# Performance work log

Hardware: AMD Instinct MI355X
Metric: run time of the kernel (lower is better)

## Reference

```python
import jax, jax.numpy as jnp
import numpy as np

EPS = 1e-5
B, C, H, W, K = 4, 512, 128, 128, 32


def setup_inputs() -> dict:
    key = jax.random.key(0)
    ks = jax.random.split(key, 12)
    std = 1.0 / ((K * C) ** 0.5)
    return {
        "x": jax.random.normal(ks[0], (B, C, H, W), jnp.float32),
        "conv_w": jax.random.normal(ks[1], (C, C), jnp.float32) * (1.0 / C ** 0.5),
        "bn2_g": jnp.ones((C,), jnp.float32),
        "bn2_b": jnp.zeros((C,), jnp.float32),
        "bn2_m": jax.random.normal(ks[2], (C,), jnp.float32) * 0.1,
        "bn2_v": jax.random.uniform(ks[3], (C,), jnp.float32) + 0.5,
        "codewords": jax.random.uniform(ks[4], (K, C), jnp.float32, -std, std),
        "scale": jax.random.uniform(ks[5], (K,), jnp.float32, -1.0, 0.0),
        "bn1_g": jnp.ones((K,), jnp.float32),
        "bn1_b": jnp.zeros((K,), jnp.float32),
        "bn1_m": jax.random.normal(ks[6], (K,), jnp.float32) * 0.1,
        "bn1_v": jax.random.uniform(ks[7], (K,), jnp.float32) + 0.5,
        "fc_w": jax.random.normal(ks[8], (C, C), jnp.float32) * (1.0 / C ** 0.5),
        "fc_b": jnp.zeros((C,), jnp.float32),
    }


def _encoding(z, codewords, scale):
    # z: [B,N,C], codewords: [K,C], scale: [K]
    # scaled L2: scale_k * ||z_n - c_k||^2, expanded to avoid the [B,N,K,C] tensor
    x2 = jnp.sum(z * z, axis=-1, keepdims=True)          # [B,N,1]
    c2 = jnp.sum(codewords * codewords, axis=-1)         # [K]
    xc = jnp.einsum('bnc,kc->bnk', z, codewords)         # [B,N,K]
    scaled_l2 = scale * (x2 - 2.0 * xc + c2)             # [B,N,K]
    assign = jax.nn.softmax(scaled_l2, axis=-1)          # softmax over codes
    # aggregate: sum_n assign[b,n,k] * (z[b,n,:] - c[k,:])
    agg = jnp.einsum('bnk,bnc->bkc', assign, z) \
        - jnp.sum(assign, axis=1)[..., None] * codewords  # [B,K,C]
    return agg


def reference(x, conv_w, bn2_g, bn2_b, bn2_m, bn2_v, codewords, scale,
              bn1_g, bn1_b, bn1_m, bn1_v, fc_w, fc_b):
    b, c, h, w = x.shape
    # encoding_project: 1x1 conv (no bias) + BN2d (eval) + ReLU
    p = jnp.einsum('bchw,oc->bohw', x, conv_w)
    p = (p - bn2_m[None, :, None, None]) * jax.lax.rsqrt(bn2_v + EPS)[None, :, None, None] \
        * bn2_g[None, :, None, None] + bn2_b[None, :, None, None]
    p = jax.nn.relu(p)
    z = p.reshape(b, c, h * w).transpose(0, 2, 1)        # [B,N,C]
    e = _encoding(z, codewords, scale)                   # [B,K,C]
    # BN1d over num_codes (eval), broadcast over channel dim, then ReLU
    e = (e - bn1_m[None, :, None]) * jax.lax.rsqrt(bn1_v + EPS)[None, :, None] \
        * bn1_g[None, :, None] + bn1_b[None, :, None]
    e = jax.nn.relu(e)
    feat = e.mean(axis=1)                                # [B,C]
    gamma = jax.nn.sigmoid(feat @ fc_w.T + fc_b)         # [B,C]
    out = jax.nn.relu(x + x * gamma[:, :, None, None])   # channel gate + residual
    return feat, out
```

## Files before the change

kernel.cpp:

```cpp
#include <hip/hip_runtime.h>
#include <cstdint>

#define EPS 1e-5f
constexpr int B = 4, C = 512, HW = 16384, K = 32;

typedef __bf16 bf16x8 __attribute__((ext_vector_type(8)));
typedef float  floatx4 __attribute__((ext_vector_type(4)));
typedef unsigned int u32;

__device__ __forceinline__ void load_lds16(const void* g, void* l) {
    __builtin_amdgcn_global_load_lds((const __attribute__((address_space(1))) u32*)g,
                                     (__attribute__((address_space(3))) u32*)l,
                                     16, 0, 0);
}

constexpr size_t Z_OFF     = 0;
constexpr size_t WBB_OFF   = 67108864;
constexpr size_t CWB_OFF   = 67633152;
constexpr size_t X2_OFF    = 67665920;
constexpr size_t C2_OFF    = 67928064;
constexpr size_t ASUM_OFF  = 67928192;
constexpr size_t PART_OFF  = 67928704;
constexpr size_t AGG_OFF   = 101483136;
constexpr size_t GAMMA_OFF = 101745280;

__global__ __launch_bounds__(256) void prep_kernel(
    const float* __restrict__ conv_w, const float* __restrict__ cw,
    __bf16* __restrict__ wbb, __bf16* __restrict__ cwb,
    float* __restrict__ c2, float* __restrict__ asum) {
    const int tid = threadIdx.x, bx = blockIdx.x;
    if (bx < 128) {
        const int idx  = bx * 256 + tid;
        const int lane = idx & 63;
        const int ks   = (idx >> 6) & 1;
        const int ii   = (idx >> 7) & 7;
        const int t    = idx >> 10;
        const float* s = conv_w + (size_t)(t * 16 + (lane & 15)) * C
                         + ii * 64 + ks * 32 + (lane >> 4) * 8;
        bf16x8 o;
        #pragma unroll
        for (int j = 0; j < 8; j++) o[j] = (__bf16)s[j];
        *(bf16x8*)&wbb[(size_t)idx * 8] = o;
    } else if (bx < 132) {
        const int idx = ((bx - 128) * 256 + tid) * 16;
        const float* s = cw + idx;
        __bf16* d = cwb + idx;
        bf16x8 o0, o1;
        #pragma unroll
        for (int j = 0; j < 8; j++) o0[j] = (__bf16)s[j];
        #pragma unroll
        for (int j = 0; j < 8; j++) o1[j] = (__bf16)s[8 + j];
        *(bf16x8*)&d[0] = o0;
        *(bf16x8*)&d[8] = o1;
    } else {
        const int k = tid >> 3, j = tid & 7;
        const float* r = cw + k * 512 + j * 64;
        float s = 0.f;
        #pragma unroll
        for (int c4 = 0; c4 < 16; c4++) {
            float4 v = *(const float4*)&r[c4 * 4];
            s += v.x * v.x + v.y * v.y + v.z * v.z + v.w * v.w;
        }
        s += __shfl_xor(s, 1); s += __shfl_xor(s, 2); s += __shfl_xor(s, 4);
        if (j == 0) c2[k] = s;
        if (tid < 128) asum[tid] = 0.f;
    }
}

__global__ __launch_bounds__(256) void conv_fused_kernel(
    const float* __restrict__ x, const __bf16* __restrict__ wbb,
    const float* __restrict__ g2, const float* __restrict__ b2,
    const float* __restrict__ m2, const float* __restrict__ v2,
    __bf16* __restrict__ z, float* __restrict__ x2g) {
    __shared__ float  XR[2][64 * 64];
    __shared__ __bf16 XA[64 * 72];
    __shared__ float  x2L[64];
    const int tid = threadIdx.x, lane = tid & 63, w = tid >> 6;
    const int l15 = lane & 15, q = lane >> 4;
    const int n0 = blockIdx.x * 64, b = blockIdx.y;
    if (tid < 64) x2L[tid] = 0.f;

    auto stage = [&](int chunk, int buf) {
        #pragma unroll
        for (int p = 0; p < 4; p++) {
            int seg = w * 4 + p;
            int cr = chunk * 64 + seg * 4 + (lane >> 4);
            const float* gp = x + ((size_t)(b * C + cr)) * HW + n0 + (lane & 15) * 4;
            load_lds16(gp, (char*)XR[buf] + seg * 1024);
        }
    };

    floatx4 acc[4][8];
    const floatx4 zv4 = {0.f, 0.f, 0.f, 0.f};
    #pragma unroll
    for (int mt = 0; mt < 4; mt++)
        #pragma unroll
        for (int ot = 0; ot < 8; ot++) acc[mt][ot] = zv4;

    stage(0, 0);
    for (int i = 0; i < 8; i++) {
        const int cur = i & 1;
        __syncthreads();
        if (i < 7) stage(i + 1, cur ^ 1);
        #pragma unroll
        for (int f = 0; f < 2; f++) {
            int id = f * 256 + tid;
            int n = id & 63, cs = id >> 6;
            bf16x8 o;
            #pragma unroll
            for (int j = 0; j < 8; j++) o[j] = (__bf16)XR[cur][(cs * 8 + j) * 64 + n];
            *(bf16x8*)&XA[n * 72 + cs * 8] = o;
        }
        asm volatile("s_waitcnt lgkmcnt(0)" ::: "memory");
        __builtin_amdgcn_sched_barrier(0);
        __builtin_amdgcn_s_barrier();
        __builtin_amdgcn_sched_barrier(0);
        #pragma unroll
        for (int ks = 0; ks < 2; ks++) {
            bf16x8 af[4], bfv[8];
            #pragma unroll
            for (int ot = 0; ot < 8; ot++)
                bfv[ot] = *(const bf16x8*)&wbb[
                    ((size_t)(((w * 8 + ot) * 8 + i) * 2 + ks) * 64 + lane) * 8];
            #pragma unroll
            for (int mt = 0; mt < 4; mt++)
                af[mt] = *(const bf16x8*)&XA[(mt * 16 + l15) * 72 + ks * 32 + q * 8];
            #pragma unroll
            for (int mt = 0; mt < 4; mt++)
                #pragma unroll
                for (int ot = 0; ot < 8; ot++)
                    acc[mt][ot] = __builtin_amdgcn_mfma_f32_16x16x32_bf16(
                        af[mt], bfv[ot], acc[mt][ot], 0, 0, 0);
        }
    }
    float s8[8], bi8[8];
    #pragma unroll
    for (int ot = 0; ot < 8; ot++) {
        int o = w * 128 + ot * 16 + l15;
        float s = g2[o] * rsqrtf(v2[o] + EPS);
        s8[ot] = s; bi8[ot] = b2[o] - m2[o] * s;
    }
    float xx[16];
    #pragma unroll
    for (int t = 0; t < 16; t++) xx[t] = 0.f;
    #pragma unroll
    for (int mt = 0; mt < 4; mt++)
        #pragma unroll
        for (int reg = 0; reg < 4; reg++) {
            int n = n0 + mt * 16 + q * 4 + reg;
            #pragma unroll
            for (int ot = 0; ot < 8; ot++) {
                float v = fmaxf(acc[mt][ot][reg] * s8[ot] + bi8[ot], 0.f);
                z[((size_t)(b * HW + n)) * C + w * 128 + ot * 16 + l15] = (__bf16)v;
                xx[mt * 4 + reg] += v * v;
            }
        }
    #pragma unroll
    for (int t = 0; t < 16; t++) {
        float v = xx[t];
        v += __shfl_xor(v, 1); v += __shfl_xor(v, 2);
        v += __shfl_xor(v, 4); v += __shfl_xor(v, 8);
        xx[t] = v;
    }
    if (l15 == 0) {
        #pragma unroll
        for (int mt = 0; mt < 4; mt++)
            #pragma unroll
            for (int reg = 0; reg < 4; reg++)
                atomicAdd(&x2L[mt * 16 + q * 4 + reg], xx[mt * 4 + reg]);
    }
    __syncthreads();
    if (tid < 64) x2g[(size_t)b * HW + n0 + tid] = x2L[tid];
}

__global__ __launch_bounds__(256) void assign_agg_kernel(
    const __bf16* __restrict__ zb, const __bf16* __restrict__ cwb,
    const float* __restrict__ scale, const float* __restrict__ c2,
    const float* __restrict__ x2g, float* __restrict__ part,
    float* __restrict__ asum) {
    __shared__ __bf16 ZT[32][536];
    __shared__ float  LG[32][33];
    __shared__ __bf16 AT[32][40];
    __shared__ float  asum_l[32];
    const int tid = threadIdx.x, lane = tid & 63, w = tid >> 6;
    const int l15 = lane & 15, q = lane >> 4;
    const int b = blockIdx.y, bx = blockIdx.x;
    if (tid < 32) asum_l[tid] = 0.f;
    float sck[8], c2k[8];
    #pragma unroll
    for (int j = 0; j < 8; j++) { sck[j] = scale[q * 8 + j]; c2k[j] = c2[q * 8 + j]; }
    const int mt_ = w >> 1, nt_ = w & 1;

    float x2r[4];
    if (w < 2) {
        #pragma unroll
        for (int s = 0; s < 4; s++)
            x2r[s] = x2g[(size_t)b * HW + bx * 128 + s * 32 + w * 16 + l15];
    }

    floatx4 agga[2][8];
    const floatx4 zv4 = {0.f, 0.f, 0.f, 0.f};
    #pragma unroll
    for (int mt = 0; mt < 2; mt++)
        #pragma unroll
        for (int ct = 0; ct < 8; ct++) agga[mt][ct] = zv4;

    bf16x8 st[8];
    #pragma unroll
    for (int p = 0; p < 8; p++) {
        int e = (p * 256 + tid) * 8;
        st[p] = *(const bf16x8*)&zb[((size_t)(b * HW + bx * 128 + (e >> 9))) * C + (e & 511)];
    }

    for (int s = 0; s < 4; s++) {
        const int nb = bx * 128 + s * 32;
        __syncthreads();
        #pragma unroll
        for (int p = 0; p < 8; p++) {
            int e = (p * 256 + tid) * 8;
            *(bf16x8*)&ZT[e >> 9][e & 511] = st[p];
        }
        if (s < 3) {
            #pragma unroll
            for (int p = 0; p < 8; p++) {
                int e = (p * 256 + tid) * 8;
                st[p] = *(const bf16x8*)&zb[
                    ((size_t)(b * HW + nb + 32 + (e >> 9))) * C + (e & 511)];
            }
        }
        asm volatile("s_waitcnt lgkmcnt(0)" ::: "memory");
        __builtin_amdgcn_sched_barrier(0);
        __builtin_amdgcn_s_barrier();
        __builtin_amdgcn_sched_barrier(0);
        floatx4 la = zv4;
        #pragma unroll
        for (int kc = 0; kc < 16; kc++) {
            bf16x8 a  = *(const bf16x8*)&cwb[(size_t)(mt_ * 16 + l15) * C + kc * 32 + q * 8];
            bf16x8 bb = *(const bf16x8*)&ZT[nt_ * 16 + l15][kc * 32 + q * 8];
            la = __builtin_amdgcn_mfma_f32_16x16x32_bf16(a, bb, la, 0, 0, 0);
        }
        #pragma unroll
        for (int r = 0; r < 4; r++)
            LG[mt_ * 16 + q * 4 + r][nt_ * 16 + l15] = la[r];
        asm volatile("s_waitcnt lgkmcnt(0)" ::: "memory");
        __builtin_amdgcn_sched_barrier(0);
        __builtin_amdgcn_s_barrier();
        __builtin_amdgcn_sched_barrier(0);
        if (w < 2) {
            int nl = w * 16 + l15;
            float lg[8];
            float mx = -1e30f;
            #pragma unroll
            for (int j = 0; j < 8; j++) {
                float t = sck[j] * (x2r[s] - 2.f * LG[q * 8 + j][nl] + c2k[j]);
                lg[j] = t; mx = fmaxf(mx, t);
            }
            mx = fmaxf(mx, __shfl_xor(mx, 16));
            mx = fmaxf(mx, __shfl_xor(mx, 32));
            float se = 0.f;
            #pragma unroll
            for (int j = 0; j < 8; j++) { lg[j] = __expf(lg[j] - mx); se += lg[j]; }
            se += __shfl_xor(se, 16);
            se += __shfl_xor(se, 32);
            float inv = 1.f / se;
            #pragma unroll
            for (int j = 0; j < 8; j++) {
                float a = lg[j] * inv;
                AT[q * 8 + j][nl] = (__bf16)a;
                lg[j] = a;
            }
            #pragma unroll
            for (int j = 0; j < 8; j++) {
                float v = lg[j];
                v += __shfl_xor(v, 1); v += __shfl_xor(v, 2);
                v += __shfl_xor(v, 4); v += __shfl_xor(v, 8);
                if (l15 == 0) atomicAdd(&asum_l[q * 8 + j], v);
            }
        }
        asm volatile("s_waitcnt lgkmcnt(0)" ::: "memory");
        __builtin_amdgcn_sched_barrier(0);
        __builtin_amdgcn_s_barrier();
        __builtin_amdgcn_sched_barrier(0);
        bf16x8 afr0 = *(const bf16x8*)&AT[l15][q * 8];
        bf16x8 afr1 = *(const bf16x8*)&AT[16 + l15][q * 8];
        #pragma unroll
        for (int ct = 0; ct < 8; ct++) {
            int c = w * 128 + ct * 16 + l15;
            bf16x8 bb;
            #pragma unroll
            for (int j = 0; j < 8; j++) bb[j] = ZT[q * 8 + j][c];
            agga[0][ct] = __builtin_amdgcn_mfma_f32_16x16x32_bf16(afr0, bb, agga[0][ct], 0, 0, 0);
            agga[1][ct] = __builtin_amdgcn_mfma_f32_16x16x32_bf16(afr1, bb, agga[1][ct], 0, 0, 0);
        }
    }
    float* pp = part + ((size_t)(b * 128 + bx) * K) * C;
    #pragma unroll
    for (int mt = 0; mt < 2; mt++)
        #pragma unroll
        for (int ct = 0; ct < 8; ct++)
            #pragma unroll
            for (int r = 0; r < 4; r++)
                pp[(size_t)(mt * 16 + q * 4 + r) * C + w * 128 + ct * 16 + l15] =
                    agga[mt][ct][r];
    __syncthreads();
    if (tid < 32) atomicAdd(&asum[b * K + tid], asum_l[tid]);
}

__global__ __launch_bounds__(128) void agg_reduce_kernel(
    const float* __restrict__ part, float* __restrict__ agg) {
    const int k = blockIdx.x, b = blockIdx.y;
    const int c = threadIdx.x * 4;
    const float* base = part + ((size_t)(b * 128) * K + k) * C + c;
    float4 s[4];
    #pragma unroll
    for (int a = 0; a < 4; a++) s[a] = {0.f, 0.f, 0.f, 0.f};
    for (int p0 = 0; p0 < 128; p0 += 16) {
        #pragma unroll
        for (int u = 0; u < 16; u++) {
            float4 v = *(const float4*)(base + (size_t)(p0 + u) * K * C);
            int a = u & 3;
            s[a].x += v.x; s[a].y += v.y; s[a].z += v.z; s[a].w += v.w;
        }
    }
    float4 r;
    r.x = (s[0].x + s[1].x) + (s[2].x + s[3].x);
    r.y = (s[0].y + s[1].y) + (s[2].y + s[3].y);
    r.z = (s[0].z + s[1].z) + (s[2].z + s[3].z);
    r.w = (s[0].w + s[1].w) + (s[2].w + s[3].w);
    *(float4*)&agg[((size_t)(b * K + k)) * C + c] = r;
}

__global__ __launch_bounds__(512) void feat_kernel(
    const float* __restrict__ cw,
    const float* __restrict__ g1, const float* __restrict__ b1,
    const float* __restrict__ m1, const float* __restrict__ v1,
    const float* __restrict__ fcw, const float* __restrict__ fcb,
    const float* __restrict__ agg, const float* __restrict__ asum,
    float* __restrict__ gamma, float* __restrict__ out_feat) {
    __shared__ float featL[C];
    const int tid = threadIdx.x;
    const int b = blockIdx.y, grp = blockIdx.x;
    float f = 0.f;
    for (int kk = 0; kk < K; kk++) {
        float s = g1[kk] * rsqrtf(v1[kk] + EPS);
        float bias = b1[kk] - m1[kk] * s;
        float e = agg[((size_t)b * K + kk) * C + tid] - asum[b * K + kk] * cw[kk * C + tid];
        f += fmaxf(e * s + bias, 0.f);
    }
    f *= (1.f / 32.f);
    if (grp == 0) out_feat[b * C + tid] = f;
    featL[tid] = f;
    __syncthreads();
    const int w = tid >> 6, l = tid & 63;
    const int cc0 = grp * 64 + w * 8;
    for (int cc = cc0; cc < cc0 + 8; cc++) {
        const float* row = &fcw[(size_t)cc * C + l * 8];
        float4 fa = *(const float4*)&featL[l * 8];
        float4 fb = *(const float4*)&featL[l * 8 + 4];
        float4 wa = *(const float4*)row;
        float4 wb = *(const float4*)(row + 4);
        float s = fa.x * wa.x + fa.y * wa.y + fa.z * wa.z + fa.w * wa.w
                + fb.x * wb.x + fb.y * wb.y + fb.z * wb.z + fb.w * wb.w;
        #pragma unroll
        for (int d = 32; d >= 1; d >>= 1) s += __shfl_xor(s, d);
        if (l == 0) gamma[b * C + cc] = 1.f / (1.f + __expf(-(s + fcb[cc])));
    }
}

__global__ __launch_bounds__(256) void gate_kernel(const float* __restrict__ x,
                                                   const float* __restrict__ gamma,
                                                   float* __restrict__ out) {
    size_t idx = (size_t)blockIdx.x * 256 + threadIdx.x;
    int bc = (int)(idx >> 12);
    float gm = 1.f + gamma[bc];
    float4 xv = ((const float4*)x)[idx];
    float4 r;
    r.x = fmaxf(xv.x * gm, 0.f);
    r.y = fmaxf(xv.y * gm, 0.f);
    r.z = fmaxf(xv.z * gm, 0.f);
    r.w = fmaxf(xv.w * gm, 0.f);
    ((float4*)out)[idx] = r;
}

extern "C" void kernel_launch(void* const* d_in, const int* in_sizes, int n_in,
                              void* d_out, int out_size, void* d_ws, size_t ws_size,
                              hipStream_t stream) {
    const float* x      = (const float*)d_in[0];
    const float* conv_w = (const float*)d_in[1];
    const float* bn2_g  = (const float*)d_in[2];
    const float* bn2_b  = (const float*)d_in[3];
    const float* bn2_m  = (const float*)d_in[4];
    const float* bn2_v  = (const float*)d_in[5];
    const float* cw     = (const float*)d_in[6];
    const float* scale  = (const float*)d_in[7];
    const float* bn1_g  = (const float*)d_in[8];
    const float* bn1_b  = (const float*)d_in[9];
    const float* bn1_m  = (const float*)d_in[10];
    const float* bn1_v  = (const float*)d_in[11];
    const float* fcw    = (const float*)d_in[12];
    const float* fcb    = (const float*)d_in[13];
    char* wsb = (char*)d_ws;
    __bf16* zbuf  = (__bf16*)(wsb + Z_OFF);
    __bf16* wbb   = (__bf16*)(wsb + WBB_OFF);
    __bf16* cwb   = (__bf16*)(wsb + CWB_OFF);
    float*  x2    = (float*)(wsb + X2_OFF);
    float*  c2    = (float*)(wsb + C2_OFF);
    float*  asum  = (float*)(wsb + ASUM_OFF);
    float*  part  = (float*)(wsb + PART_OFF);
    float*  agg   = (float*)(wsb + AGG_OFF);
    float*  gamma = (float*)(wsb + GAMMA_OFF);
    float* out = (float*)d_out;

    prep_kernel<<<133, 256, 0, stream>>>(conv_w, cw, wbb, cwb, c2, asum);
    conv_fused_kernel<<<dim3(256, 4), 256, 0, stream>>>(
        x, wbb, bn2_g, bn2_b, bn2_m, bn2_v, zbuf, x2);
    assign_agg_kernel<<<dim3(128, 4), 256, 0, stream>>>(
        zbuf, cwb, scale, c2, x2, part, asum);
    agg_reduce_kernel<<<dim3(32, 4), 128, 0, stream>>>(part, agg);
    feat_kernel<<<dim3(8, 4), 512, 0, stream>>>(cw, bn1_g, bn1_b, bn1_m, bn1_v,
                                                fcw, fcb, agg, asum, gamma, out);
    gate_kernel<<<32768, 256, 0, stream>>>(x, gamma, out + B * C);
}
```

Baseline: 397.8 us.

## Fuse conv projection with assignment and aggregation, keeping z tile in LDS

Result: no change. 396.3 us (-0.4%).

```diff
diff --git a/kernel.cpp b/kernel.cpp
--- a/kernel.cpp
+++ b/kernel.cpp
@@ -14,15 +14,13 @@
                                      16, 0, 0);
 }
 
-constexpr size_t Z_OFF     = 0;
+constexpr size_t PART_OFF  = 0;
 constexpr size_t WBB_OFF   = 67108864;
 constexpr size_t CWB_OFF   = 67633152;
-constexpr size_t X2_OFF    = 67665920;
+constexpr size_t AGG_OFF   = 101483136;
+constexpr size_t GAMMA_OFF = 101745280;
 constexpr size_t C2_OFF    = 67928064;
 constexpr size_t ASUM_OFF  = 67928192;
-constexpr size_t PART_OFF  = 67928704;
-constexpr size_t AGG_OFF   = 101483136;
-constexpr size_t GAMMA_OFF = 101745280;
 
 __global__ __launch_bounds__(256) void prep_kernel(
     const float* __restrict__ conv_w, const float* __restrict__ cw,
@@ -67,18 +65,31 @@
     }
 }
 
-__global__ __launch_bounds__(256) void conv_fused_kernel(
+__global__ __launch_bounds__(256) void conv_assign_kernel(
     const float* __restrict__ x, const __bf16* __restrict__ wbb,
+    const __bf16* __restrict__ cwb,
     const float* __restrict__ g2, const float* __restrict__ b2,
     const float* __restrict__ m2, const float* __restrict__ v2,
-    __bf16* __restrict__ z, float* __restrict__ x2g) {
-    __shared__ float  XR[2][64 * 64];
-    __shared__ __bf16 XA[64 * 72];
-    __shared__ float  x2L[64];
+    const float* __restrict__ scale, const float* __restrict__ c2,
+    float* __restrict__ part, float* __restrict__ asum) {
+    __shared__ __align__(16) char smem[79872];
+    float*  XR     = (float*)smem;
+    __bf16* XA     = (__bf16*)(smem + 32768);
+    __bf16* ZT     = (__bf16*)smem;
+    float*  LG     = (float*)(smem + 66560);
+    __bf16* AT     = (__bf16*)(smem + 74880);
+    float*  x2L    = (float*)(smem + 79488);
+    float*  asum_l = (float*)(smem + 79744);
+
     const int tid = threadIdx.x, lane = tid & 63, w = tid >> 6;
     const int l15 = lane & 15, q = lane >> 4;
-    const int n0 = blockIdx.x * 64, b = blockIdx.y;
+    const int bx = blockIdx.x, b = blockIdx.y;
+    const int n0 = bx * 64;
     if (tid < 64) x2L[tid] = 0.f;
+    if (tid < 32) asum_l[tid] = 0.f;
+    float sck[8], c2k[8];
+    #pragma unroll
+    for (int j = 0; j < 8; j++) { sck[j] = scale[q * 8 + j]; c2k[j] = c2[q * 8 + j]; }
 
     auto stage = [&](int chunk, int buf) {
         #pragma unroll
@@ -86,7 +97,7 @@
             int seg = w * 4 + p;
             int cr = chunk * 64 + seg * 4 + (lane >> 4);
             const float* gp = x + ((size_t)(b * C + cr)) * HW + n0 + (lane & 15) * 4;
-            load_lds16(gp, (char*)XR[buf] + seg * 1024);
+            load_lds16(gp, (char*)XR + buf * 16384 + seg * 1024);
         }
     };
 
@@ -108,7 +119,8 @@
             int n = id & 63, cs = id >> 6;
             bf16x8 o;
             #pragma unroll
-            for (int j = 0; j < 8; j++) o[j] = (__bf16)XR[cur][(cs * 8 + j) * 64 + n];
+            for (int j = 0; j < 8; j++)
+                o[j] = (__bf16)XR[cur * 4096 + (cs * 8 + j) * 64 + n];
             *(bf16x8*)&XA[n * 72 + cs * 8] = o;
         }
         asm volatile("s_waitcnt lgkmcnt(0)" ::: "memory");
@@ -133,6 +145,8 @@
                         af[mt], bfv[ot], acc[mt][ot], 0, 0, 0);
         }
     }
+    __syncthreads();
+
     float s8[8], bi8[8];
     #pragma unroll
     for (int ot = 0; ot < 8; ot++) {
@@ -147,11 +161,11 @@
     for (int mt = 0; mt < 4; mt++)
         #pragma unroll
         for (int reg = 0; reg < 4; reg++) {
-            int n = n0 + mt * 16 + q * 4 + reg;
+            int n = mt * 16 + q * 4 + reg;
             #pragma unroll
             for (int ot = 0; ot < 8; ot++) {
                 float v = fmaxf(acc[mt][ot][reg] * s8[ot] + bi8[ot], 0.f);
-                z[((size_t)(b * HW + n)) * C + w * 128 + ot * 16 + l15] = (__bf16)v;
+                ZT[n * 520 + w * 128 + ot * 16 + l15] = (__bf16)v;
                 xx[mt * 4 + reg] += v * v;
             }
         }
@@ -170,138 +184,87 @@
                 atomicAdd(&x2L[mt * 16 + q * 4 + reg], xx[mt * 4 + reg]);
     }
     __syncthreads();
-    if (tid < 64) x2g[(size_t)b * HW + n0 + tid] = x2L[tid];
-}
-
-__global__ __launch_bounds__(256) void assign_agg_kernel(
-    const __bf16* __restrict__ zb, const __bf16* __restrict__ cwb,
-    const float* __restrict__ scale, const float* __restrict__ c2,
-    const float* __restrict__ x2g, float* __restrict__ part,
-    float* __restrict__ asum) {
-    __shared__ __bf16 ZT[32][536];
-    __shared__ float  LG[32][33];
-    __shared__ __bf16 AT[32][40];
-    __shared__ float  asum_l[32];
-    const int tid = threadIdx.x, lane = tid & 63, w = tid >> 6;
-    const int l15 = lane & 15, q = lane >> 4;
-    const int b = blockIdx.y, bx = blockIdx.x;
-    if (tid < 32) asum_l[tid] = 0.f;
-    float sck[8], c2k[8];
-    #pragma unroll
-    for (int j = 0; j < 8; j++) { sck[j] = scale[q * 8 + j]; c2k[j] = c2[q * 8 + j]; }
-    const int mt_ = w >> 1, nt_ = w & 1;
-
-    float x2r[4];
-    if (w < 2) {
-        #pragma unroll
-        for (int s = 0; s < 4; s++)
-            x2r[s] = x2g[(size_t)b * HW + bx * 128 + s * 32 + w * 16 + l15];
-    }
-
-    floatx4 agga[2][8];
-    const floatx4 zv4 = {0.f, 0.f, 0.f, 0.f};
-    #pragma unroll
-    for (int mt = 0; mt < 2; mt++)
-        #pragma unroll
-        for (int ct = 0; ct < 8; ct++) agga[mt][ct] = zv4;
-
-    bf16x8 st[8];
-    #pragma unroll
-    for (int p = 0; p < 8; p++) {
-        int e = (p * 256 + tid) * 8;
-        st[p] = *(const bf16x8*)&zb[((size_t)(b * HW + bx * 128 + (e >> 9))) * C + (e & 511)];
-    }
-
-    for (int s = 0; s < 4; s++) {
-        const int nb = bx * 128 + s * 32;
-        __syncthreads();
-        #pragma unroll
-        for (int p = 0; p < 8; p++) {
-            int e = (p * 256 + tid) * 8;
-            *(bf16x8*)&ZT[e >> 9][e & 511] = st[p];
-        }
-        if (s < 3) {
-            #pragma unroll
-            for (int p = 0; p < 8; p++) {
-                int e = (p * 256 + tid) * 8;
-                st[p] = *(const bf16x8*)&zb[
-                    ((size_t)(b * HW + nb + 32 + (e >> 9))) * C + (e & 511)];
-            }
-        }
-        asm volatile("s_waitcnt lgkmcnt(0)" ::: "memory");
-        __builtin_amdgcn_sched_barrier(0);
-        __builtin_amdgcn_s_barrier();
-        __builtin_amdgcn_sched_barrier(0);
-        floatx4 la = zv4;
-        #pragma unroll
-        for (int kc = 0; kc < 16; kc++) {
-            bf16x8 a  = *(const bf16x8*)&cwb[(size_t)(mt_ * 16 + l15) * C + kc * 32 + q * 8];
-            bf16x8 bb = *(const bf16x8*)&ZT[nt_ * 16 + l15][kc * 32 + q * 8];
-            la = __builtin_amdgcn_mfma_f32_16x16x32_bf16(a, bb, la, 0, 0, 0);
-        }
-        #pragma unroll
-        for (int r = 0; r < 4; r++)
-            LG[mt_ * 16 + q * 4 + r][nt_ * 16 + l15] = la[r];
-        asm volatile("s_waitcnt lgkmcnt(0)" ::: "memory");
-        __builtin_amdgcn_sched_barrier(0);
-        __builtin_amdgcn_s_barrier();
-        __builtin_amdgcn_sched_barrier(0);
-        if (w < 2) {
-            int nl = w * 16 + l15;
-            float lg[8];
-            float mx = -1e30f;
-            #pragma unroll
-            for (int j = 0; j < 8; j++) {
-                float t = sck[j] * (x2r[s] - 2.f * LG[q * 8 + j][nl] + c2k[j]);
-                lg[j] = t; mx = fmaxf(mx, t);
-            }
-            mx = fmaxf(mx, __shfl_xor(mx, 16));
-            mx = fmaxf(mx, __shfl_xor(mx, 32));
-            float se = 0.f;
-            #pragma unroll
-            for (int j = 0; j < 8; j++) { lg[j] = __expf(lg[j] - mx); se += lg[j]; }
-            se += __shfl_xor(se, 16);
-            se += __shfl_xor(se, 32);
-            float inv = 1.f / se;
-            #pragma unroll
-            for (int j = 0; j < 8; j++) {
-                float a = lg[j] * inv;
-                AT[q * 8 + j][nl] = (__bf16)a;
-                lg[j] = a;
-            }
-            #pragma unroll
-            for (int j = 0; j < 8; j++) {
-                float v = lg[j];
-                v += __shfl_xor(v, 1); v += __shfl_xor(v, 2);
-                v += __shfl_xor(v, 4); v += __shfl_xor(v, 8);
-                if (l15 == 0) atomicAdd(&asum_l[q * 8 + j], v);
-            }
-        }
-        asm volatile("s_waitcnt lgkmcnt(0)" ::: "memory");
-        __builtin_amdgcn_sched_barrier(0);
-        __builtin_amdgcn_s_barrier();
-        __builtin_amdgcn_sched_barrier(0);
-        bf16x8 afr0 = *(const bf16x8*)&AT[l15][q * 8];
-        bf16x8 afr1 = *(const bf16x8*)&AT[16 + l15][q * 8];
-        #pragma unroll
-        for (int ct = 0; ct < 8; ct++) {
-            int c = w * 128 + ct * 16 + l15;
-            bf16x8 bb;
-            #pragma unroll
-            for (int j = 0; j < 8; j++) bb[j] = ZT[q * 8 + j][c];
-            agga[0][ct] = __builtin_amdgcn_mfma_f32_16x16x32_bf16(afr0, bb, agga[0][ct], 0, 0, 0);
-            agga[1][ct] = __builtin_amdgcn_mfma_f32_16x16x32_bf16(afr1, bb, agga[1][ct], 0, 0, 0);
-        }
-    }
-    float* pp = part + ((size_t)(b * 128 + bx) * K) * C;
-    #pragma unroll
-    for (int mt = 0; mt < 2; mt++)
-        #pragma unroll
-        for (int ct = 0; ct < 8; ct++)
-            #pragma unroll
-            for (int r = 0; r < 4; r++)
-                pp[(size_t)(mt * 16 + q * 4 + r) * C + w * 128 + ct * 16 + l15] =
-                    agga[mt][ct][r];
+
+    const int kh = w >> 1, nq0 = w & 1;
+    floatx4 la0 = zv4, la1 = zv4;
+    #pragma unroll
+    for (int kc = 0; kc < 16; kc++) {
+        bf16x8 a  = *(const bf16x8*)&cwb[(size_t)(kh * 16 + l15) * C + kc * 32 + q * 8];
+        bf16x8 b0 = *(const bf16x8*)&ZT[(nq0 * 16 + l15) * 520 + kc * 32 + q * 8];
+        bf16x8 b1 = *(const bf16x8*)&ZT[((nq0 + 2) * 16 + l15) * 520 + kc * 32 + q * 8];
+        la0 = __builtin_amdgcn_mfma_f32_16x16x32_bf16(a, b0, la0, 0, 0, 0);
+        la1 = __builtin_amdgcn_mfma_f32_16x16x32_bf16(a, b1, la1, 0, 0, 0);
+    }
+    #pragma unroll
+    for (int r = 0; r < 4; r++) {
+        LG[(kh * 16 + q * 4 + r) * 65 + nq0 * 16 + l15]       = la0[r];
+        LG[(kh * 16 + q * 4 + r) * 65 + (nq0 + 2) * 16 + l15] = la1[r];
+    }
+    __syncthreads();
+
+    {
+        int nl = w * 16 + l15;
+        float x2v = x2L[nl];
+        float lg[8];
+        float mx = -1e30f;
+        #pragma unroll
+        for (int j = 0; j < 8; j++) {
+            float t = sck[j] * (x2v - 2.f * LG[(q * 8 + j) * 65 + nl] + c2k[j]);
+            lg[j] = t; mx = fmaxf(mx, t);
+        }
+        mx = fmaxf(mx, __shfl_xor(mx, 16));
+        mx = fmaxf(mx, __shfl_xor(mx, 32));
+        float se = 0.f;
+        #pragma unroll
+        for (int j = 0; j < 8; j++) { lg[j] = __expf(lg[j] - mx); se += lg[j]; }
+        se += __shfl_xor(se, 16);
+        se += __shfl_xor(se, 32);
+        float inv = 1.f / se;
+        #pragma unroll
+        for (int j = 0; j < 8; j++) {
+            float a = lg[j] * inv;
+            AT[(q * 8 + j) * 72 + nl] = (__bf16)a;
+            lg[j] = a;
+        }
+        #pragma unroll
+        for (int j = 0; j < 8; j++) {
+            float v = lg[j];
+            v += __shfl_xor(v, 1); v += __shfl_xor(v, 2);
+            v += __shfl_xor(v, 4); v += __shfl_xor(v, 8);
+            if (l15 == 0) atomicAdd(&asum_l[q * 8 + j], v);
+        }
+    }
+    __syncthreads();
+
+    bf16x8 af00 = *(const bf16x8*)&AT[l15 * 72 + q * 8];
+    bf16x8 af01 = *(const bf16x8*)&AT[l15 * 72 + 32 + q * 8];
+    bf16x8 af10 = *(const bf16x8*)&AT[(16 + l15) * 72 + q * 8];
+    bf16x8 af11 = *(const bf16x8*)&AT[(16 + l15) * 72 + 32 + q * 8];
+    floatx4 agga0[8], agga1[8];
+    #pragma unroll
+    for (int ct = 0; ct < 8; ct++) { agga0[ct] = zv4; agga1[ct] = zv4; }
+    #pragma unroll
+    for (int ct = 0; ct < 8; ct++) {
+        int c = w * 128 + ct * 16 + l15;
+        bf16x8 b0, b1;
+        #pragma unroll
+        for (int j = 0; j < 8; j++) {
+            b0[j] = ZT[(q * 8 + j) * 520 + c];
+            b1[j] = ZT[(32 + q * 8 + j) * 520 + c];
+        }
+        agga0[ct] = __builtin_amdgcn_mfma_f32_16x16x32_bf16(af00, b0, agga0[ct], 0, 0, 0);
+        agga0[ct] = __builtin_amdgcn_mfma_f32_16x16x32_bf16(af01, b1, agga0[ct], 0, 0, 0);
+        agga1[ct] = __builtin_amdgcn_mfma_f32_16x16x32_bf16(af10, b0, agga1[ct], 0, 0, 0);
+        agga1[ct] = __builtin_amdgcn_mfma_f32_16x16x32_bf16(af11, b1, agga1[ct], 0, 0, 0);
+    }
+    float* pp = part + ((size_t)(b * 256 + bx) * K) * C;
+    #pragma unroll
+    for (int ct = 0; ct < 8; ct++)
+        #pragma unroll
+        for (int r = 0; r < 4; r++) {
+            pp[(size_t)(q * 4 + r) * C + w * 128 + ct * 16 + l15]        = agga0[ct][r];
+            pp[(size_t)(16 + q * 4 + r) * C + w * 128 + ct * 16 + l15]   = agga1[ct][r];
+        }
     __syncthreads();
     if (tid < 32) atomicAdd(&asum[b * K + tid], asum_l[tid]);
 }
@@ -310,11 +273,11 @@
     const float* __restrict__ part, float* __restrict__ agg) {
     const int k = blockIdx.x, b = blockIdx.y;
     const int c = threadIdx.x * 4;
-    const float* base = part + ((size_t)(b * 128) * K + k) * C + c;
+    const float* base = part + ((size_t)(b * 256) * K + k) * C + c;
     float4 s[4];
     #pragma unroll
     for (int a = 0; a < 4; a++) s[a] = {0.f, 0.f, 0.f, 0.f};
-    for (int p0 = 0; p0 < 128; p0 += 16) {
+    for (int p0 = 0; p0 < 256; p0 += 16) {
         #pragma unroll
         for (int u = 0; u < 16; u++) {
             float4 v = *(const float4*)(base + (size_t)(p0 + u) * K * C);
@@ -400,22 +363,18 @@
     const float* fcw    = (const float*)d_in[12];
     const float* fcb    = (const float*)d_in[13];
     char* wsb = (char*)d_ws;
-    __bf16* zbuf  = (__bf16*)(wsb + Z_OFF);
+    float*  part  = (float*)(wsb + PART_OFF);
     __bf16* wbb   = (__bf16*)(wsb + WBB_OFF);
     __bf16* cwb   = (__bf16*)(wsb + CWB_OFF);
-    float*  x2    = (float*)(wsb + X2_OFF);
     float*  c2    = (float*)(wsb + C2_OFF);
     float*  asum  = (float*)(wsb + ASUM_OFF);
-    float*  part  = (float*)(wsb + PART_OFF);
     float*  agg   = (float*)(wsb + AGG_OFF);
     float*  gamma = (float*)(wsb + GAMMA_OFF);
     float* out = (float*)d_out;
 
     prep_kernel<<<133, 256, 0, stream>>>(conv_w, cw, wbb, cwb, c2, asum);
-    conv_fused_kernel<<<dim3(256, 4), 256, 0, stream>>>(
-        x, wbb, bn2_g, bn2_b, bn2_m, bn2_v, zbuf, x2);
-    assign_agg_kernel<<<dim3(128, 4), 256, 0, stream>>>(
-        zbuf, cwb, scale, c2, x2, part, asum);
+    conv_assign_kernel<<<dim3(256, 4), 256, 0, stream>>>(
+        x, wbb, cwb, bn2_g, bn2_b, bn2_m, bn2_v, scale, c2, part, asum);
     agg_reduce_kernel<<<dim3(32, 4), 128, 0, stream>>>(part, agg);
     feat_kernel<<<dim3(8, 4), 512, 0, stream>>>(cw, bn1_g, bn1_b, bn1_m, bn1_v,
                                                 fcw, fcb, agg, asum, gamma, out);
```
